# Performance work log

Measured on AMD Instinct MI355X. Metric: run time of the kernel, lower is better.

The kernel has to match this reference:

```python
import jax, jax.numpy as jnp
import numpy as np

B = 256          # batch
MID = 16384      # mid_siz
OUT = 16384      # out_siz
C = 16           # channel_siz
NLVL = 8         # nlvl (== klvl here since floor(log2(OUT/2))=13 >= 8)
MIDF = MID >> NLVL   # mid_filter_siz = 64
OUTF = OUT >> NLVL   # out_filter_siz = 64
NB = 1 << NLVL       # 256 leaf branches
STD = 0.5


def setup_inputs() -> dict:
    key = jax.random.key(0)
    ks = jax.random.split(key, 6)
    in_data = jax.random.normal(ks[0], (B, MID, 2), jnp.float32)
    # learned parameters (buildRand: normal(0, 0.5) filters, zero biases)
    mid_dense = jax.random.normal(ks[1], (1, MID, 2), jnp.float32) * STD
    in_filter = jax.random.normal(ks[2], (MIDF, 1, C), jnp.float32) * STD   # conv1d [width,in,out]
    in_bias = jnp.zeros((C,), jnp.float32)
    # level lvl (1..NLVL) uses filters[lvl-1, :2**lvl]; padded to NB branches
    filters = jax.random.normal(ks[3], (NLVL, NB, 2, C, C), jnp.float32) * STD
    biases = jnp.zeros((NLVL, NB, C), jnp.float32)
    fea_dense = jax.random.normal(ks[4], (NB, C, OUTF), jnp.float32) * STD
    return dict(in_data=in_data, mid_dense=mid_dense, in_filter=in_filter,
                in_bias=in_bias, filters=filters, biases=biases, fea_dense=fea_dense)


def reference(in_data, mid_dense, in_filter, in_bias, filters, biases, fea_dense):
    # elementwise modulation then split real/imag channels: (B, 2, MID)
    x = jnp.moveaxis(in_data * mid_dense, -1, 1)
    # level-0 conv1d: kernel MIDF, stride MIDF//2 -> overlapping half-windows.
    # Split signal into half-width chunks h; window t = [h[t], h[t+1]].
    half = MIDF // 2
    h = x.reshape(B, 2, MID // half, half)                 # (B,2,512,32)
    W1 = in_filter[:half, 0, :]                            # (32,C)
    W2 = in_filter[half:, 0, :]
    s = jnp.einsum('bisw,wc->bisc', h[:, :, :-1], W1) \
        + jnp.einsum('bisw,wc->bisc', h[:, :, 1:], W2)
    s = jax.nn.relu(s + in_bias)                           # (B,2,2^(n+1)-1,C)
    state = s[:, :, None]                                  # (B,2,nb=1,L,C)
    # butterfly tree: each level doubles branches; conv kernel=2, stride=2, VALID
    for lvl in range(1, NLVL + 1):
        nb = 1 << lvl
        p = jnp.repeat(state, 2, axis=2)                   # child itk <- parent itk//2
        L = p.shape[3]                                     # odd: 2^(n+1-lvl+1)-1
        xw = p[:, :, :, :L - 1, :].reshape(B, 2, nb, (L - 1) // 2, 2, C)
        W = filters[lvl - 1, :nb]                          # (nb,2,C,C)
        bb = biases[lvl - 1, :nb]                          # (nb,C)
        state = jax.nn.relu(
            jnp.einsum('bintkc,nkcd->bintd', xw, W) + bb[None, None, :, None, :])
    feat = state[:, :, :, 0, :]                            # (B,2,NB,C): L==1 at last level
    outp = jnp.einsum('binc,ncf->binf', feat, fea_dense)   # per-branch dense projection
    R = outp[:, 0].reshape(B, OUT // 2, 2)
    I = outp[:, 1].reshape(B, OUT // 2, 2)
    out_data = ((R[:, :, 0] - I[:, :, 1]) / MID).reshape(B, OUT // 2, 1)
    return out_data, R[:, :, 1]
```

## Files before the change

kernel.cpp:

```cpp
#include <hip/hip_runtime.h>
#include <hip/hip_bf16.h>


#define OUT_HALF 2097152

typedef __attribute__((ext_vector_type(4))) float f32x4;
typedef __attribute__((ext_vector_type(8))) short s16x8;

__device__ __forceinline__ uint fsw(uint a) {
    return a ^ ((((a >> 6) ^ (a >> 8)) & 3u) << 4);
}
__device__ __forceinline__ ushort bfr(float f) {
    __hip_bfloat16 h = __float2bfloat16(f);
    union { __hip_bfloat16 h; ushort u; } cv; cv.h = h; return cv.u;
}
__device__ __forceinline__ uint pk(float a, float b) {
    return (uint)bfr(a) | ((uint)bfr(b) << 16);
}

__device__ __forceinline__ void tree_level(
    char* smb, const int lane, const int wave,
    uint AOff, uint NOff, int lgR, int lgNP, int nTiles,
    uint WOff, int wnb, uint LBOff, int bnb)
{
    const int m  = lane & 15;
    const int kg = lane >> 4;
    const int lgTPP = lgR - 4;
    for (int at = wave; at < nTiles; at += 4) {
        const int p  = at >> lgTPP;
        const int tc = at & ((1 << lgTPP) - 1);
        const int np = p & ((1 << lgNP) - 1);
        const int ii = p >> lgNP;
        s16x8 af = *(const s16x8*)(smb + AOff + (p << (lgR + 6)) +
                                   fsw((uint)((tc * 16 + m) * 64 + kg * 16)));
#pragma unroll
        for (int sib = 0; sib < 2; sib++) {
            const int nl = 2 * np + sib;
            s16x8 bf = *(const s16x8*)(smb + WOff +
                         fsw((uint)((wnb + nl) * 1024 + m * 64 + kg * 16)));
            float bv = *(const float*)(smb + LBOff + ((bnb + nl) * 16 + m) * 4);
            f32x4 acc = {bv, bv, bv, bv};
            acc = __builtin_amdgcn_mfma_f32_16x16x32_bf16(af, bf, acc, 0, 0, 0);
            const int p2 = (ii << (lgNP + 1)) + nl;
            const uint wb = NOff + (p2 << (lgR + 5));
            const int r2 = tc * 8 + kg * 2;
            *(uint*)(smb + wb + fsw((uint)(r2 * 64 + m * 4))) =
                pk(fmaxf(acc.x, 0.f), fmaxf(acc.y, 0.f));
            *(uint*)(smb + wb + fsw((uint)((r2 + 1) * 64 + m * 4))) =
                pk(fmaxf(acc.z, 0.f), fmaxf(acc.w, 0.f));
        }
    }
}

__global__ __launch_bounds__(256, 4)
void ibf_A(const float* __restrict__ in_data, const float* __restrict__ mid_dense,
           const float* __restrict__ in_filter, const float* __restrict__ in_bias,
           const float* __restrict__ filters, const float* __restrict__ biases,
           uint* __restrict__ S3)
{
    __shared__ __align__(16) char smb[29760];
    const int tid = threadIdx.x, lane = tid & 63, wave = tid >> 6;
    const int b = blockIdx.x;
    const int th = blockIdx.y >> 1;
    const int i  = blockIdx.y & 1;

    {
        const float4* inb = (const float4*)in_data + (size_t)b * 8192 + th * 2048;
        const float4* mdb = (const float4*)mid_dense + th * 2048;
        for (int mp = tid; mp < 2064; mp += 256) {
            float4 iv = inb[mp], mv = mdb[mp];
            float xa = i ? iv.y * mv.y : iv.x * mv.x;
            float xb = i ? iv.w * mv.w : iv.z * mv.z;
            *(uint*)(smb + fsw((uint)(mp * 4))) = pk(xa, xb);
        }
    }
    for (int t = tid; t < 3584; t += 256) {
        int nidx = t >> 8, r = t & 255, d = r & 15, c = r >> 4;
        int lvl = (nidx < 2) ? 1 : ((nidx < 6) ? 2 : 3);
        int n = nidx - ((1 << lvl) - 2);
        const float* src = filters + (size_t)(lvl - 1) * 131072 + n * 512 + c * 16 + d;
        *(uint*)(smb + 12416 + fsw((uint)(nidx * 1024 + d * 64 + c * 4))) = pk(src[0], src[256]);
    }
    for (int t = tid; t < 512; t += 256) {
        int c = t >> 5, w2 = t & 31;
        *(uint*)(smb + 26752 + fsw((uint)(c * 128 + w2 * 4))) =
            pk(in_filter[(2 * w2) * 16 + c], in_filter[(2 * w2 + 1) * 16 + c]);
    }
    if (tid < 240) {
        float v;
        if (tid < 224) {
            int nidx = tid >> 4;
            int lvl = (nidx < 2) ? 1 : ((nidx < 6) ? 2 : 3);
            int n = nidx - ((1 << lvl) - 2);
            v = biases[(size_t)(lvl - 1) * 4096 + n * 16 + (tid & 15)];
        } else v = in_bias[tid - 224];
        *(float*)(smb + 28800 + tid * 4) = v;
    }
    __syncthreads();

    {
        const int m = lane & 15, kg = lane >> 4;
        s16x8 b0 = *(const s16x8*)(smb + 26752 + fsw((uint)(m * 128 + kg * 16)));
        s16x8 b1 = *(const s16x8*)(smb + 26752 + fsw((uint)(m * 128 + 64 + kg * 16)));
        float bv = *(const float*)(smb + 28800 + (224 + m) * 4);
        for (int at = wave; at < 8; at += 4) {
            int tc = at;
            s16x8 a0 = *(const s16x8*)(smb + fsw((uint)((tc * 16 + m) * 64 + kg * 16)));
            s16x8 a1 = *(const s16x8*)(smb + fsw((uint)((tc * 16 + m) * 64 + 64 + kg * 16)));
            f32x4 acc = {bv, bv, bv, bv};
            acc = __builtin_amdgcn_mfma_f32_16x16x32_bf16(a0, b0, acc, 0, 0, 0);
            acc = __builtin_amdgcn_mfma_f32_16x16x32_bf16(a1, b1, acc, 0, 0, 0);
            int r2 = tc * 8 + kg * 2;
            *(uint*)(smb + 8320 + fsw((uint)(r2 * 64 + m * 4))) =
                pk(fmaxf(acc.x, 0.f), fmaxf(acc.y, 0.f));
            *(uint*)(smb + 8320 + fsw((uint)((r2 + 1) * 64 + m * 4))) =
                pk(fmaxf(acc.z, 0.f), fmaxf(acc.w, 0.f));
        }
    }
    __syncthreads();
    tree_level(smb, lane, wave, 8320, 0,    6, 0, 4, 12416, 0, 28800, 0);
    __syncthreads();
    tree_level(smb, lane, wave, 0,    8320, 5, 1, 4, 12416, 2, 28800, 2);
    __syncthreads();
    {
        const int m = lane & 15, kg = lane >> 4;
        for (int at = wave; at < 4; at += 4) {
            s16x8 af = *(const s16x8*)(smb + 8320 + (at << 10) + fsw((uint)(m * 64 + kg * 16)));
#pragma unroll
            for (int sib = 0; sib < 2; sib++) {
                int n3 = 2 * at + sib;
                s16x8 bf = *(const s16x8*)(smb + 12416 +
                             fsw((uint)((6 + n3) * 1024 + m * 64 + kg * 16)));
                float bv = *(const float*)(smb + 28800 + ((6 + n3) * 16 + m) * 4);
                f32x4 acc = {bv, bv, bv, bv};
                acc = __builtin_amdgcn_mfma_f32_16x16x32_bf16(af, bf, acc, 0, 0, 0);
                int bi = 2 * b + i;
                int t4 = th * 8 + kg * 2;
                uint idx = ((uint)(n3 * 512 + bi) * 16 + t4) * 16 + m;
                S3[idx]      = pk(fmaxf(acc.x, 0.f), fmaxf(acc.y, 0.f));
                S3[idx + 16] = pk(fmaxf(acc.z, 0.f), fmaxf(acc.w, 0.f));
            }
        }
    }
}

__global__ __launch_bounds__(256, 2)
void ibf_B(const float* __restrict__ filters, const float* __restrict__ biases,
           const uint* __restrict__ S3, char* __restrict__ S8)
{
    __shared__ __align__(16) char smb[61312];
    const int tid = threadIdx.x, lane = tid & 63, wave = tid >> 6;
    const int n3 = blockIdx.x, chunk = blockIdx.y;

    {
        const char* src = (const char*)S3 + ((size_t)n3 * 512 + chunk * 8) * 1024;
        for (int ci = tid; ci < 512; ci += 256)
            *(float4*)(smb + fsw((uint)(ci * 16))) = *(const float4*)(src + ci * 16);
    }
    for (int t = tid; t < 992; t += 256) {
        int nidx = t >> 4, q = nidx + 2;
        int l3 = 31 - __clz(q);
        int nl = q - (1 << l3);
        int gn = (n3 << l3) + nl;
        *(float*)(smb + 57344 + t * 4) = biases[(size_t)(l3 + 2) * 4096 + gn * 16 + (t & 15)];
    }
    auto stage_w = [&](int l3) {
        int NL = 1 << l3;
        const float* fb = filters + (size_t)(l3 + 2) * 131072;
        for (int t = tid; t < NL * 256; t += 256) {
            int nl = t >> 8, r = t & 255, d = r & 15, c = r >> 4;
            const float* src = fb + (size_t)((n3 << l3) + nl) * 512 + c * 16 + d;
            *(uint*)(smb + 24576 + fsw((uint)(nl * 1024 + d * 64 + c * 4))) = pk(src[0], src[256]);
        }
    };
    stage_w(1);
    __syncthreads();
    tree_level(smb, lane, wave, 0,    8192, 7, 0, 8, 24576, 0, 57344, 0);
    __syncthreads();
    stage_w(2);
    __syncthreads();
    tree_level(smb, lane, wave, 8192, 0,    6, 1, 8, 24576, 0, 57344, 2);
    __syncthreads();
    stage_w(3);
    __syncthreads();
    tree_level(smb, lane, wave, 0,    8192, 5, 2, 8, 24576, 0, 57344, 6);
    __syncthreads();
    stage_w(4);
    __syncthreads();
    tree_level(smb, lane, wave, 8192, 0,    4, 3, 8, 24576, 0, 57344, 14);
    __syncthreads();
    stage_w(5);
    __syncthreads();
    {
        const int m = lane & 15, kg = lane >> 4;
        for (int at = wave; at < 16; at += 4) {
            s16x8 af = *(const s16x8*)(smb + at * 512 + fsw((uint)(m * 64 + kg * 16)));
#pragma unroll
            for (int sib = 0; sib < 2; sib++) {
                int nl = 2 * at + sib;
                s16x8 bf = *(const s16x8*)(smb + 24576 +
                             fsw((uint)(nl * 1024 + m * 64 + kg * 16)));
                float bv = *(const float*)(smb + 57344 + ((30 + nl) * 16 + m) * 4);
                f32x4 acc = {bv, bv, bv, bv};
                acc = __builtin_amdgcn_mfma_f32_16x16x32_bf16(af, bf, acc, 0, 0, 0);
                if (kg < 2) {
                    float v[4] = {fmaxf(acc.x, 0.f), fmaxf(acc.y, 0.f),
                                  fmaxf(acc.z, 0.f), fmaxf(acc.w, 0.f)};
#pragma unroll
                    for (int j = 0; j < 4; j++)
                        *(ushort*)(smb + 16384 + nl * 256 + (kg * 4 + j) * 32 + m * 2) = bfr(v[j]);
                }
            }
        }
    }
    __syncthreads();
    {
        float4* dst = (float4*)(S8 + (size_t)(n3 * 64 + chunk) * 8192);
        for (int ci = tid; ci < 512; ci += 256)
            dst[ci] = *(const float4*)(smb + 16384 + ci * 16);
    }
}

__global__ __launch_bounds__(256, 4)
void ibf_C(const float* __restrict__ fea_dense, const char* __restrict__ S8,
           float* __restrict__ out)
{
    __shared__ ushort FEb[1024];
    const int tid = threadIdx.x, lane = tid & 63, wave = tid >> 6;
    const int n8g = blockIdx.x, q = blockIdx.y;
    const int n3 = n8g >> 5, n8l = n8g & 31;

    for (int idx = tid; idx < 1024; idx += 256) {
        int c = idx >> 6, u = idx & 63;
        FEb[u * 16 + c] = bfr(fea_dense[(size_t)n8g * 1024 + idx]);
    }
    __syncthreads();

    const int m = lane & 15, kg = lane >> 4;
    s16x8 bfrg[4];
#pragma unroll
    for (int ut = 0; ut < 4; ut++) {
        if (kg < 2) bfrg[ut] = *(const s16x8*)(FEb + (ut * 16 + m) * 16 + kg * 8);
        else        bfrg[ut] = (s16x8){0, 0, 0, 0, 0, 0, 0, 0};
    }
    for (int w = 0; w < 2; w++) {
        const int tile  = q * 8 + wave * 2 + w;
        const int birow = tile * 16 + m;
        s16x8 af = {0, 0, 0, 0, 0, 0, 0, 0};
        if (kg < 2)
            af = *(const s16x8*)(S8 + ((size_t)(n3 * 64 + (birow >> 3)) * 32 + n8l) * 256
                                 + (birow & 7) * 32 + kg * 16);
        const int b0  = (tile * 16 + kg * 4) >> 1;
        const bool odd = (m & 1);
#pragma unroll
        for (int ut = 0; ut < 4; ut++) {
            f32x4 acc = {0.f, 0.f, 0.f, 0.f};
            acc = __builtin_amdgcn_mfma_f32_16x16x32_bf16(af, bfrg[ut], acc, 0, 0, 0);
            float sy = __shfl_xor(acc.y, 1);
            float sw = __shfl_xor(acc.w, 1);
            const int g = n8g * 32 + ut * 8 + (m >> 1);
            float v0 = odd ? acc.x : (acc.x - sy) * (1.f / 16384.f);
            float v1 = odd ? acc.z : (acc.z - sw) * (1.f / 16384.f);
            size_t off = (odd ? (size_t)OUT_HALF : (size_t)0) + (size_t)g;
            out[(size_t)b0 * 8192 + off]       = v0;
            out[(size_t)(b0 + 1) * 8192 + off] = v1;
        }
    }
}

extern "C" void kernel_launch(void* const* d_in, const int* in_sizes, int n_in,
                              void* d_out, int out_size, void* d_ws, size_t ws_size,
                              hipStream_t stream) {
    const float* in_data   = (const float*)d_in[0];
    const float* mid_dense = (const float*)d_in[1];
    const float* in_filter = (const float*)d_in[2];
    const float* in_bias   = (const float*)d_in[3];
    const float* filters   = (const float*)d_in[4];
    const float* biases    = (const float*)d_in[5];
    const float* fea_dense = (const float*)d_in[6];
    float* out = (float*)d_out;
    uint* S3   = (uint*)d_ws;
    char* S8   = (char*)d_ws + (4 << 20);

    ibf_A<<<dim3(256, 4), 256, 0, stream>>>(in_data, mid_dense, in_filter, in_bias,
                                            filters, biases, S3);
    ibf_B<<<dim3(8, 64), 256, 0, stream>>>(filters, biases, S3, S8);
    ibf_C<<<dim3(256, 4), 256, 0, stream>>>(fea_dense, S8, out);
}
```

Before: 41.16 us.

## Load tree-level filter fragments directly into registers in ibf_B

Each level's bf16 filter and bias fragments in ibf_B are now loaded straight from global memory into registers, prefetched one level ahead, instead of being staged through LDS with stage_w plus extra barriers. The generic tree_level calls are replaced with specialised unrolled per-level MFMA code. LDS use drops from about 61 KB to 24 KB, which may allow more resident blocks, and several syncthreads are removed. The cost is more registers for the prefetched fragments and uncoalesced strided global loads for the filters.

```diff
diff --git a/kernel.cpp b/kernel.cpp
--- a/kernel.cpp
+++ b/kernel.cpp
@@ -148,68 +148,157 @@
 void ibf_B(const float* __restrict__ filters, const float* __restrict__ biases,
            const uint* __restrict__ S3, char* __restrict__ S8)
 {
-    __shared__ __align__(16) char smb[61312];
+    __shared__ __align__(16) char smb[24576];
     const int tid = threadIdx.x, lane = tid & 63, wave = tid >> 6;
     const int n3 = blockIdx.x, chunk = blockIdx.y;
-
+    const int m = lane & 15, kg = lane >> 4;
+
+    const float* FB1 = filters + (size_t)3 * 131072 + ((size_t)(n3 << 1)) * 512;
+    const float* FB2 = filters + (size_t)4 * 131072 + ((size_t)(n3 << 2)) * 512;
+    const float* FB3 = filters + (size_t)5 * 131072 + ((size_t)(n3 << 3)) * 512;
+    const float* FB4 = filters + (size_t)6 * 131072 + ((size_t)(n3 << 4)) * 512;
+    const float* FB5 = filters + (size_t)7 * 131072 + ((size_t)(n3 << 5)) * 512;
+    const float* BB1 = biases + (size_t)3 * 4096 + (n3 << 1) * 16;
+    const float* BB2 = biases + (size_t)4 * 4096 + (n3 << 2) * 16;
+    const float* BB3 = biases + (size_t)5 * 4096 + (n3 << 3) * 16;
+    const float* BB4 = biases + (size_t)6 * 4096 + (n3 << 4) * 16;
+    const float* BB5 = biases + (size_t)7 * 4096 + (n3 << 5) * 16;
+
+#define LDFRAG(dst, fb, nl)                                                  \
+    {                                                                        \
+        const float* s_ = (fb) + (nl) * 512 + m;                             \
+        _Pragma("unroll")                                                    \
+        for (int c4 = 0; c4 < 4; c4++) {                                     \
+            int c_ = kg * 4 + c4;                                            \
+            (&(dst).x)[c4] = pk(s_[c_ * 16], s_[256 + c_ * 16]);             \
+        }                                                                    \
+    }
+
+    uint4 f4[2], f5[4];
+    float b4[2], b5[4];
+    LDFRAG(f4[0], FB1, 0); LDFRAG(f4[1], FB1, 1);
+    b4[0] = BB1[m]; b4[1] = BB1[16 + m];
+#pragma unroll
+    for (int s = 0; s < 4; s++) { LDFRAG(f5[s], FB2, s); b5[s] = BB2[s * 16 + m]; }
     {
         const char* src = (const char*)S3 + ((size_t)n3 * 512 + chunk * 8) * 1024;
         for (int ci = tid; ci < 512; ci += 256)
             *(float4*)(smb + fsw((uint)(ci * 16))) = *(const float4*)(src + ci * 16);
     }
-    for (int t = tid; t < 992; t += 256) {
-        int nidx = t >> 4, q = nidx + 2;
-        int l3 = 31 - __clz(q);
-        int nl = q - (1 << l3);
-        int gn = (n3 << l3) + nl;
-        *(float*)(smb + 57344 + t * 4) = biases[(size_t)(l3 + 2) * 4096 + gn * 16 + (t & 15)];
-    }
-    auto stage_w = [&](int l3) {
-        int NL = 1 << l3;
-        const float* fb = filters + (size_t)(l3 + 2) * 131072;
-        for (int t = tid; t < NL * 256; t += 256) {
-            int nl = t >> 8, r = t & 255, d = r & 15, c = r >> 4;
-            const float* src = fb + (size_t)((n3 << l3) + nl) * 512 + c * 16 + d;
-            *(uint*)(smb + 24576 + fsw((uint)(nl * 1024 + d * 64 + c * 4))) = pk(src[0], src[256]);
-        }
-    };
-    stage_w(1);
-    __syncthreads();
-    tree_level(smb, lane, wave, 0,    8192, 7, 0, 8, 24576, 0, 57344, 0);
-    __syncthreads();
-    stage_w(2);
-    __syncthreads();
-    tree_level(smb, lane, wave, 8192, 0,    6, 1, 8, 24576, 0, 57344, 2);
-    __syncthreads();
-    stage_w(3);
-    __syncthreads();
-    tree_level(smb, lane, wave, 0,    8192, 5, 2, 8, 24576, 0, 57344, 6);
-    __syncthreads();
-    stage_w(4);
-    __syncthreads();
-    tree_level(smb, lane, wave, 8192, 0,    4, 3, 8, 24576, 0, 57344, 14);
-    __syncthreads();
-    stage_w(5);
-    __syncthreads();
-    {
-        const int m = lane & 15, kg = lane >> 4;
-        for (int at = wave; at < 16; at += 4) {
-            s16x8 af = *(const s16x8*)(smb + at * 512 + fsw((uint)(m * 64 + kg * 16)));
-#pragma unroll
-            for (int sib = 0; sib < 2; sib++) {
-                int nl = 2 * at + sib;
-                s16x8 bf = *(const s16x8*)(smb + 24576 +
-                             fsw((uint)(nl * 1024 + m * 64 + kg * 16)));
-                float bv = *(const float*)(smb + 57344 + ((30 + nl) * 16 + m) * 4);
-                f32x4 acc = {bv, bv, bv, bv};
-                acc = __builtin_amdgcn_mfma_f32_16x16x32_bf16(af, bf, acc, 0, 0, 0);
-                if (kg < 2) {
-                    float v[4] = {fmaxf(acc.x, 0.f), fmaxf(acc.y, 0.f),
-                                  fmaxf(acc.z, 0.f), fmaxf(acc.w, 0.f)};
-#pragma unroll
-                    for (int j = 0; j < 4; j++)
-                        *(ushort*)(smb + 16384 + nl * 256 + (kg * 4 + j) * 32 + m * 2) = bfr(v[j]);
-                }
+    __syncthreads();
+
+    uint4 f6[4];
+    float b6[4];
+    {
+        const int n0 = (wave >> 1) * 2;
+        LDFRAG(f6[0], FB3, n0);     b6[0] = BB3[(n0) * 16 + m];
+        LDFRAG(f6[1], FB3, n0 + 1); b6[1] = BB3[(n0 + 1) * 16 + m];
+        LDFRAG(f6[2], FB3, n0 + 4); b6[2] = BB3[(n0 + 4) * 16 + m];
+        LDFRAG(f6[3], FB3, n0 + 5); b6[3] = BB3[(n0 + 5) * 16 + m];
+    }
+#pragma unroll
+    for (int t2 = 0; t2 < 2; t2++) {
+        const int tc = wave + t2 * 4;
+        s16x8 af = *(const s16x8*)(smb + fsw((uint)((tc * 16 + m) * 64 + kg * 16)));
+#pragma unroll
+        for (int sib = 0; sib < 2; sib++) {
+            f32x4 acc = {b4[sib], b4[sib], b4[sib], b4[sib]};
+            acc = __builtin_amdgcn_mfma_f32_16x16x32_bf16(af, *(const s16x8*)&f4[sib], acc, 0, 0, 0);
+            const uint wb = 8192u + (uint)sib * 4096u;
+            const int r2 = tc * 8 + kg * 2;
+            *(uint*)(smb + wb + fsw((uint)(r2 * 64 + m * 4))) = pk(fmaxf(acc.x, 0.f), fmaxf(acc.y, 0.f));
+            *(uint*)(smb + wb + fsw((uint)((r2 + 1) * 64 + m * 4))) = pk(fmaxf(acc.z, 0.f), fmaxf(acc.w, 0.f));
+        }
+    }
+    __syncthreads();
+
+    uint4 f7[4];
+    float b7[4];
+    {
+        LDFRAG(f7[0], FB4, 2 * wave);     b7[0] = BB4[(2 * wave) * 16 + m];
+        LDFRAG(f7[1], FB4, 2 * wave + 1); b7[1] = BB4[(2 * wave + 1) * 16 + m];
+        LDFRAG(f7[2], FB4, 2 * wave + 8); b7[2] = BB4[(2 * wave + 8) * 16 + m];
+        LDFRAG(f7[3], FB4, 2 * wave + 9); b7[3] = BB4[(2 * wave + 9) * 16 + m];
+    }
+#pragma unroll
+    for (int t2 = 0; t2 < 2; t2++) {
+        const int at = wave + t2 * 4;
+        const int p = at >> 2, tc = at & 3;
+        s16x8 af = *(const s16x8*)(smb + 8192 + p * 4096 + fsw((uint)((tc * 16 + m) * 64 + kg * 16)));
+#pragma unroll
+        for (int sib = 0; sib < 2; sib++) {
+            const int nl = 2 * p + sib;
+            f32x4 acc = {b5[nl], b5[nl], b5[nl], b5[nl]};
+            acc = __builtin_amdgcn_mfma_f32_16x16x32_bf16(af, *(const s16x8*)&f5[nl], acc, 0, 0, 0);
+            const uint wb = (uint)nl * 2048u;
+            const int r2 = tc * 8 + kg * 2;
+            *(uint*)(smb + wb + fsw((uint)(r2 * 64 + m * 4))) = pk(fmaxf(acc.x, 0.f), fmaxf(acc.y, 0.f));
+            *(uint*)(smb + wb + fsw((uint)((r2 + 1) * 64 + m * 4))) = pk(fmaxf(acc.z, 0.f), fmaxf(acc.w, 0.f));
+        }
+    }
+    __syncthreads();
+
+    uint4 f8[8];
+    float b8[8];
+#pragma unroll
+    for (int t4 = 0; t4 < 4; t4++) {
+        const int at = wave + 4 * t4;
+        LDFRAG(f8[2 * t4],     FB5, 2 * at);     b8[2 * t4]     = BB5[(2 * at) * 16 + m];
+        LDFRAG(f8[2 * t4 + 1], FB5, 2 * at + 1); b8[2 * t4 + 1] = BB5[(2 * at + 1) * 16 + m];
+    }
+#pragma unroll
+    for (int t2 = 0; t2 < 2; t2++) {
+        const int at = wave + t2 * 4;
+        const int p = at >> 1, tc = at & 1;
+        s16x8 af = *(const s16x8*)(smb + p * 2048 + fsw((uint)((tc * 16 + m) * 64 + kg * 16)));
+#pragma unroll
+        for (int sib = 0; sib < 2; sib++) {
+            const int nl = 2 * p + sib;
+            const int fi = t2 * 2 + sib;
+            f32x4 acc = {b6[fi], b6[fi], b6[fi], b6[fi]};
+            acc = __builtin_amdgcn_mfma_f32_16x16x32_bf16(af, *(const s16x8*)&f6[fi], acc, 0, 0, 0);
+            const uint wb = 8192u + (uint)nl * 1024u;
+            const int r2 = tc * 8 + kg * 2;
+            *(uint*)(smb + wb + fsw((uint)(r2 * 64 + m * 4))) = pk(fmaxf(acc.x, 0.f), fmaxf(acc.y, 0.f));
+            *(uint*)(smb + wb + fsw((uint)((r2 + 1) * 64 + m * 4))) = pk(fmaxf(acc.z, 0.f), fmaxf(acc.w, 0.f));
+        }
+    }
+    __syncthreads();
+
+#pragma unroll
+    for (int t2 = 0; t2 < 2; t2++) {
+        const int p = wave + t2 * 4;
+        s16x8 af = *(const s16x8*)(smb + 8192 + p * 1024 + fsw((uint)(m * 64 + kg * 16)));
+#pragma unroll
+        for (int sib = 0; sib < 2; sib++) {
+            const int nl = 2 * p + sib;
+            const int fi = t2 * 2 + sib;
+            f32x4 acc = {b7[fi], b7[fi], b7[fi], b7[fi]};
+            acc = __builtin_amdgcn_mfma_f32_16x16x32_bf16(af, *(const s16x8*)&f7[fi], acc, 0, 0, 0);
+            const uint wb = (uint)nl * 512u;
+            const int r2 = kg * 2;
+            *(uint*)(smb + wb + fsw((uint)(r2 * 64 + m * 4))) = pk(fmaxf(acc.x, 0.f), fmaxf(acc.y, 0.f));
+            *(uint*)(smb + wb + fsw((uint)((r2 + 1) * 64 + m * 4))) = pk(fmaxf(acc.z, 0.f), fmaxf(acc.w, 0.f));
+        }
+    }
+    __syncthreads();
+
+#pragma unroll
+    for (int t4 = 0; t4 < 4; t4++) {
+        const int at = wave + 4 * t4;
+        s16x8 af = *(const s16x8*)(smb + at * 512 + fsw((uint)(m * 64 + kg * 16)));
+#pragma unroll
+        for (int sib = 0; sib < 2; sib++) {
+            const int nl = 2 * at + sib;
+            const int fi = t4 * 2 + sib;
+            f32x4 acc = {b8[fi], b8[fi], b8[fi], b8[fi]};
+            acc = __builtin_amdgcn_mfma_f32_16x16x32_bf16(af, *(const s16x8*)&f8[fi], acc, 0, 0, 0);
+            if (kg < 2) {
+                float v[4] = {fmaxf(acc.x, 0.f), fmaxf(acc.y, 0.f),
+                              fmaxf(acc.z, 0.f), fmaxf(acc.w, 0.f)};
+#pragma unroll
+                for (int j = 0; j < 4; j++)
+                    *(ushort*)(smb + 16384 + nl * 256 + (kg * 4 + j) * 32 + m * 2) = bfr(v[j]);
             }
         }
     }
@@ -219,6 +308,7 @@
         for (int ci = tid; ci < 512; ci += 256)
             dst[ci] = *(const float4*)(smb + 16384 + ci * 16);
     }
+#undef LDFRAG
 }
 
 __global__ __launch_bounds__(256, 4)
```

Result: no change. 40.55 us (-1.5%).
